# Performance work log

Hardware: AMD Instinct MI355X
Metric: run time of the kernel (lower is better)

## Reference

```python
import jax, jax.numpy as jnp
import numpy as np

HID = 1024; NH = 4; HD = HID // NH; KS = 4; C = 64; EPS = 1e-05
B = 4; L = 4096


def setup_inputs():
    key = jax.random.key(0)
    ks = jax.random.split(key, 9)
    return {
        "x": jax.random.normal(ks[0], (B, L, HID), jnp.float32),
        "Wq": jax.random.normal(ks[1], (HID, HID), jnp.float32) * 0.02,
        "Wk": jax.random.normal(ks[2], (HID, HID), jnp.float32) * 0.02,
        "Wv": jax.random.normal(ks[3], (HID, HID), jnp.float32) * 0.02,
        "Wb": jax.random.normal(ks[4], (HID, NH), jnp.float32) * 0.02,
        "conv_q": jax.random.normal(ks[5], (HID, 1, KS), jnp.float32) * 0.5,
        "conv_k": jax.random.normal(ks[6], (HID, 1, KS), jnp.float32) * 0.5,
        "conv_v": jax.random.normal(ks[7], (HID, 1, KS), jnp.float32) * 0.5,
        "g": jnp.ones((HD,), jnp.float32),
        "Wo": jax.random.normal(ks[8], (HID, HID), jnp.float32) * 0.02,
    }


def _causal_dwconv(x, w):
    # x: (B, L, Ch); w: (Ch, 1, K). Depthwise causal conv (left pad K-1) + SiLU,
    # equivalent to torch Conv1d(padding=K-1) followed by right-truncation.
    xc = jnp.moveaxis(x, 1, 2)  # (B, Ch, L)
    y = jax.lax.conv_general_dilated(
        xc, w, window_strides=(1,), padding=[(w.shape[-1] - 1, 0)],
        dimension_numbers=("NCH", "OIH", "NCH"), feature_group_count=w.shape[0])
    return jnp.moveaxis(jax.nn.silu(y), 1, 2)


def _forward(x, Wq, Wk, Wv, Wb, conv_q, conv_k, conv_v, g, Wo):
    Bx, Lx, _ = x.shape
    N = Lx // C  # num chunks (L chosen divisible by C)
    q = _causal_dwconv(x @ Wq, conv_q).reshape(Bx, Lx, NH, HD)
    k = _causal_dwconv(x @ Wk, conv_k).reshape(Bx, Lx, NH, HD)
    v = _causal_dwconv(x @ Wv, conv_v).reshape(Bx, Lx, NH, HD)
    # kq_norm: L2-normalize each head vector over head_dim
    q = q / jnp.linalg.norm(q, axis=-1, keepdims=True)
    k = k / jnp.linalg.norm(k, axis=-1, keepdims=True)
    beta = jax.nn.sigmoid(x @ Wb)  # (B, L, H)
    Q = q.reshape(Bx, N, C, NH, HD)
    K = k.reshape(Bx, N, C, NH, HD)
    V = v.reshape(Bx, N, C, NH, HD)
    bta = beta.reshape(Bx, N, C, NH, 1)
    Kb = K * bta
    Vb = V * bta
    # T = eye(C) - sum_h tril(Kb_h @ K_h^T, -1)  (T shared across heads, as in source)
    A = jnp.einsum("bnihd,bnjhd->bnij", Kb, K)
    T0 = jnp.eye(C, dtype=x.dtype) - jnp.tril(A, -1)
    col = jnp.arange(C)

    def body(i, T):
        # Replicates: T[:,:,i,:i] += (T[:,:,i,:,None] * T[:,:,:,:i]).sum(-2)
        row = jax.lax.dynamic_slice_in_dim(T, i, 1, axis=2)[:, :, 0]  # (B,N,C)
        acc = jnp.einsum("bnj,bnjc->bnc", row, T)
        new_row = jnp.where(col < i, row + acc, row)
        return jax.lax.dynamic_update_slice_in_dim(T, new_row[:, :, None, :], i, axis=2)

    T = jax.lax.fori_loop(1, C, body, T0)
    W = jnp.einsum("bnij,bnjhd->bnihd", T, Kb)
    U = jnp.einsum("bnij,bnjhd->bnihd", T, Vb)

    def chunk_step(S, inp):
        q_i, k_i, w_i, u0 = inp  # each (B, C, H, D)
        # source einsum 'bchd,bhdd->bchd' extracts the diagonal of S
        Sd = jnp.diagonal(S, axis1=-2, axis2=-1)  # (B, H, D)
        u_i = u0 - w_i * Sd[:, None]
        o_inter = q_i * Sd[:, None]
        # source: einsum('bchd,bchd->bc', q, k).tril() -- tril over the (B, C) matrix
        A_i = jnp.tril(jnp.einsum("bchd,bchd->bc", q_i, k_i))
        o_intra = A_i[:, :, None, None] * u_i
        S = S + jnp.einsum("bchd,bche->bhde", k_i, u_i)
        return S, o_inter + o_intra

    xs = tuple(jnp.moveaxis(a, 1, 0) for a in (Q, K, W, U))  # (N, B, C, H, D)
    S0 = jnp.zeros((Bx, NH, HD, HD), x.dtype)
    S, O = jax.lax.scan(chunk_step, S0, xs)
    o = jnp.moveaxis(O, 0, 1).reshape(Bx, Lx, NH, HD)
    # RMSNorm over head_dim with learned scale g
    o = o * jax.lax.rsqrt(jnp.mean(o * o, axis=-1, keepdims=True) + EPS) * g
    out = o.reshape(Bx, Lx, NH * HD) @ Wo
    return out, S


def reference(x, Wq, Wk, Wv, Wb, conv_q, conv_k, conv_v, g, Wo):
    return _forward(x, Wq, Wk, Wv, Wb, conv_q, conv_k, conv_v, g, Wo)
```

## Files before the change

### kernel.cpp

```cpp
#include <hip/hip_runtime.h>
#include <hip/hip_bf16.h>

#define HID 1024
#define NH 4
#define HD 256
#define NCH 64
#define BB 4
#define LL 4096
#define ROWS (BB*LL)
#define SSIZE (BB*NH*HD*HD)

typedef __hip_bfloat16 bf16;
typedef __attribute__((ext_vector_type(8))) short short8;
typedef __attribute__((ext_vector_type(4))) float f32x4;

struct u16x4 { unsigned short x, y, z, w; };

__device__ __forceinline__ float bfu2f(unsigned short u) {
  return __uint_as_float(((unsigned int)u) << 16);
}
__device__ __forceinline__ unsigned short f2bfu(float f) {
  unsigned int x = __float_as_uint(f);
  return (unsigned short)((x + 0x7FFFu + ((x >> 16) & 1u)) >> 16);
}
__device__ __forceinline__ float ldv(const float* p) { return *p; }
__device__ __forceinline__ float ldv(const bf16* p) { return bfu2f(*(const unsigned short*)p); }
__device__ __forceinline__ float4 ld4(const float* p) { return *(const float4*)p; }
__device__ __forceinline__ float4 ld4(const bf16* p) {
  u16x4 u = *(const u16x4*)p;
  return make_float4(bfu2f(u.x), bfu2f(u.y), bfu2f(u.z), bfu2f(u.w));
}
__device__ __forceinline__ void st4(float* p, float4 v) { *(float4*)p = v; }
__device__ __forceinline__ void st4(bf16* p, float4 v) {
  u16x4 u; u.x = f2bfu(v.x); u.y = f2bfu(v.y); u.z = f2bfu(v.z); u.w = f2bfu(v.w);
  *(u16x4*)p = u;
}

typedef const __attribute__((address_space(1))) unsigned int* gptr_t;
typedef __attribute__((address_space(3))) unsigned int* lptr_t;
__device__ __forceinline__ void gload16(const void* g, void* l) {
  __builtin_amdgcn_global_load_lds((gptr_t)g, (lptr_t)l, 16, 0, 0);
}

__global__ __launch_bounds__(256)
void beta_kernel(const float* __restrict__ x, const float* __restrict__ Wb,
                 float* __restrict__ beta) {
  const int wave = threadIdx.x >> 6, lane = threadIdx.x & 63;
  const int m = (blockIdx.x << 2) + wave;
  const float* xr = x + (size_t)m * HID;
  float a0 = 0.f, a1 = 0.f, a2 = 0.f, a3 = 0.f;
#pragma unroll
  for (int it = 0; it < 16; ++it) {
    int kk = lane + (it << 6);
    float xv = xr[kk];
    float4 w = *(const float4*)&Wb[kk << 2];
    a0 += xv * w.x; a1 += xv * w.y; a2 += xv * w.z; a3 += xv * w.w;
  }
#pragma unroll
  for (int off = 32; off; off >>= 1) {
    a0 += __shfl_xor(a0, off); a1 += __shfl_xor(a1, off);
    a2 += __shfl_xor(a2, off); a3 += __shfl_xor(a3, off);
  }
  if (lane == 0) {
    float4 r;
    r.x = 1.f / (1.f + expf(-a0)); r.y = 1.f / (1.f + expf(-a1));
    r.z = 1.f / (1.f + expf(-a2)); r.w = 1.f / (1.f + expf(-a3));
    *(float4*)&beta[m << 2] = r;
  }
}

__global__ __launch_bounds__(256)
void convX2_kernel(const float* __restrict__ x, bf16* __restrict__ hi,
                   bf16* __restrict__ lo) {
  size_t i = ((size_t)blockIdx.x * 256 + threadIdx.x) << 2;
  float4 v = *(const float4*)&x[i];
  u16x4 h; h.x = f2bfu(v.x); h.y = f2bfu(v.y); h.z = f2bfu(v.z); h.w = f2bfu(v.w);
  *(u16x4*)&hi[i] = h;
  u16x4 l;
  l.x = f2bfu(v.x - bfu2f(h.x)); l.y = f2bfu(v.y - bfu2f(h.y));
  l.z = f2bfu(v.z - bfu2f(h.z)); l.w = f2bfu(v.w - bfu2f(h.w));
  *(u16x4*)&lo[i] = l;
}

__global__ __launch_bounds__(256)
void convT_kernel(const float* __restrict__ W, unsigned short* __restrict__ Wt) {
  __shared__ unsigned short t[64][68];
  const int kt = blockIdx.x << 6, nt = blockIdx.y << 6;
  const int tid = threadIdx.x;
#pragma unroll
  for (int i = 0; i < 16; ++i) {
    int idx = tid + (i << 8);
    int r = idx >> 6, c = idx & 63;
    t[r][c] = f2bfu(W[(size_t)(kt + r) * HID + nt + c]);
  }
  __syncthreads();
#pragma unroll
  for (int i = 0; i < 16; ++i) {
    int idx = tid + (i << 8);
    int n = idx >> 6, kk = idx & 63;
    Wt[(size_t)(nt + n) * HID + kt + kk] = t[kk][n];
  }
}

__global__ __launch_bounds__(256)
void convT2_kernel(const float* __restrict__ W, unsigned short* __restrict__ Wht,
                   unsigned short* __restrict__ Wlt) {
  __shared__ float t[64][65];
  const int kt = blockIdx.x << 6, nt = blockIdx.y << 6;
  const int tid = threadIdx.x;
#pragma unroll
  for (int i = 0; i < 16; ++i) {
    int idx = tid + (i << 8);
    int r = idx >> 6, c = idx & 63;
    t[r][c] = W[(size_t)(kt + r) * HID + nt + c];
  }
  __syncthreads();
#pragma unroll
  for (int i = 0; i < 16; ++i) {
    int idx = tid + (i << 8);
    int n = idx >> 6, kk = idx & 63;
    float v = t[kk][n];
    unsigned short h = f2bfu(v);
    Wht[(size_t)(nt + n) * HID + kt + kk] = h;
    Wlt[(size_t)(nt + n) * HID + kt + kk] = f2bfu(v - bfu2f(h));
  }
}

__global__ __launch_bounds__(256)
void ktrans_kernel(const float* __restrict__ k, unsigned short* __restrict__ kt) {
  __shared__ float t[64][65];
  const int r0 = blockIdx.x << 6, c0 = blockIdx.y << 6;
  const int tid = threadIdx.x;
#pragma unroll
  for (int i = 0; i < 16; ++i) {
    int idx = tid + (i << 8);
    int rr = idx >> 6, cc = idx & 63;
    t[rr][cc] = k[(size_t)(r0 + rr) * HID + c0 + cc];
  }
  __syncthreads();
#pragma unroll
  for (int i = 0; i < 16; ++i) {
    int idx = tid + (i << 8);
    int cc = idx >> 6, rr = idx & 63;
    kt[(size_t)(c0 + cc) * ROWS + r0 + rr] = f2bfu(t[rr][cc]);
  }
}

__global__ __launch_bounds__(256)
void mfma_gemm(const unsigned short* __restrict__ A,
               const unsigned short* __restrict__ Bt, float* __restrict__ C) {
  __shared__ unsigned short Asl[128 * 32];
  __shared__ unsigned short Bsl[128 * 32];
  const int tid = threadIdx.x;
  const int wave = tid >> 6, lane = tid & 63;
  const int m0 = blockIdx.x << 7, n0 = blockIdx.y << 7;
  const int wr = wave >> 1, wc = wave & 1;
  f32x4 acc[4][4] = {};
  const int cA = (wave << 6) + lane;
  for (int k0 = 0; k0 < HID; k0 += 32) {
#pragma unroll
    for (int i = 0; i < 2; ++i) {
      int c = cA + (i << 8);
      int row = c >> 2, ko = (c & 3) << 3;
      gload16(&A[(size_t)(m0 + row) * HID + k0 + ko],
              &Asl[(size_t)((i << 8) + (wave << 6)) * 8]);
      gload16(&Bt[(size_t)(n0 + row) * HID + k0 + ko],
              &Bsl[(size_t)((i << 8) + (wave << 6)) * 8]);
    }
    __syncthreads();
    short8 af[4], bfr[4];
#pragma unroll
    for (int f = 0; f < 4; ++f) {
      int ra = (wr << 6) + (f << 4) + (lane & 15);
      af[f] = *(const short8*)&Asl[ra * 32 + ((lane >> 4) << 3)];
      int rb = (wc << 6) + (f << 4) + (lane & 15);
      bfr[f] = *(const short8*)&Bsl[rb * 32 + ((lane >> 4) << 3)];
    }
#pragma unroll
    for (int i = 0; i < 4; ++i)
#pragma unroll
      for (int j = 0; j < 4; ++j)
        acc[i][j] = __builtin_amdgcn_mfma_f32_16x16x32_bf16(af[i], bfr[j],
                                                            acc[i][j], 0, 0, 0);
    __syncthreads();
  }
#pragma unroll
  for (int i = 0; i < 4; ++i) {
    int r0 = m0 + (wr << 6) + (i << 4) + ((lane >> 4) << 2);
#pragma unroll
    for (int j = 0; j < 4; ++j) {
      int c0 = n0 + (wc << 6) + (j << 4) + (lane & 15);
#pragma unroll
      for (int r = 0; r < 4; ++r)
        C[(size_t)(r0 + r) * HID + c0] = acc[i][j][r];
    }
  }
}

__global__ __launch_bounds__(256)
void mfma_gemm3(const unsigned short* __restrict__ Ah_,
                const unsigned short* __restrict__ Al_,
                const unsigned short* __restrict__ Bh_,
                const unsigned short* __restrict__ Bl_,
                float* __restrict__ C) {
  __shared__ unsigned short Ah[128 * 32];
  __shared__ unsigned short Al[128 * 32];
  __shared__ unsigned short Bh[128 * 32];
  __shared__ unsigned short Bl[128 * 32];
  const int tid = threadIdx.x;
  const int wave = tid >> 6, lane = tid & 63;
  const int m0 = blockIdx.x << 7, n0 = blockIdx.y << 7;
  const int wr = wave >> 1, wc = wave & 1;
  f32x4 acc[4][4] = {};
  const int cA = (wave << 6) + lane;
  for (int k0 = 0; k0 < HID; k0 += 32) {
#pragma unroll
    for (int i = 0; i < 2; ++i) {
      int c = cA + (i << 8);
      int row = c >> 2, ko = (c & 3) << 3;
      size_t ga = (size_t)(m0 + row) * HID + k0 + ko;
      size_t gb = (size_t)(n0 + row) * HID + k0 + ko;
      size_t ldst = (size_t)((i << 8) + (wave << 6)) * 8;
      gload16(&Ah_[ga], &Ah[ldst]);
      gload16(&Al_[ga], &Al[ldst]);
      gload16(&Bh_[gb], &Bh[ldst]);
      gload16(&Bl_[gb], &Bl[ldst]);
    }
    __syncthreads();
    short8 ah[4], al[4], bh[4], bl[4];
#pragma unroll
    for (int f = 0; f < 4; ++f) {
      int ra = ((wr << 6) + (f << 4) + (lane & 15)) * 32 + ((lane >> 4) << 3);
      ah[f] = *(const short8*)&Ah[ra];
      al[f] = *(const short8*)&Al[ra];
      int rb = ((wc << 6) + (f << 4) + (lane & 15)) * 32 + ((lane >> 4) << 3);
      bh[f] = *(const short8*)&Bh[rb];
      bl[f] = *(const short8*)&Bl[rb];
    }
#pragma unroll
    for (int i = 0; i < 4; ++i)
#pragma unroll
      for (int j = 0; j < 4; ++j) {
        f32x4 a = acc[i][j];
        a = __builtin_amdgcn_mfma_f32_16x16x32_bf16(al[i], bh[j], a, 0, 0, 0);
        a = __builtin_amdgcn_mfma_f32_16x16x32_bf16(ah[i], bl[j], a, 0, 0, 0);
        a = __builtin_amdgcn_mfma_f32_16x16x32_bf16(ah[i], bh[j], a, 0, 0, 0);
        acc[i][j] = a;
      }
    __syncthreads();
  }
#pragma unroll
  for (int i = 0; i < 4; ++i) {
    int r0 = m0 + (wr << 6) + (i << 4) + ((lane >> 4) << 2);
#pragma unroll
    for (int j = 0; j < 4; ++j) {
      int c0 = n0 + (wc << 6) + (j << 4) + (lane & 15);
#pragma unroll
      for (int r = 0; r < 4; ++r)
        C[(size_t)(r0 + r) * HID + c0] = acc[i][j][r];
    }
  }
}

__global__ __launch_bounds__(256)
void mfma_gemmS(const unsigned short* __restrict__ At,
                const unsigned short* __restrict__ Bt,
                float* __restrict__ Spart, int ngroups) {
  __shared__ unsigned short Asl[128 * 32];
  __shared__ unsigned short Bsl[128 * 32];
  const int tid = threadIdx.x;
  const int wave = tid >> 6, lane = tid & 63;
  const int m0 = blockIdx.x << 7, n0 = blockIdx.y << 7;
  const int bh = blockIdx.z / ngroups;
  const int ng = blockIdx.z % ngroups;
  const int b = bh >> 2, h = bh & 3;
  const size_t kbase = (size_t)b * LL + (size_t)ng * (LL / ngroups);
  const int wr = wave >> 1, wc = wave & 1;
  f32x4 acc[4][4] = {};
  const int cA = (wave << 6) + lane;
  for (int k0 = 0; k0 < LL / ngroups; k0 += 32) {
#pragma unroll
    for (int i = 0; i < 2; ++i) {
      int c = cA + (i << 8);
      int row = c >> 2, ko = (c & 3) << 3;
      gload16(&At[((size_t)(h * HD + m0 + row)) * ROWS + kbase + k0 + ko],
              &Asl[(size_t)((i << 8) + (wave << 6)) * 8]);
      gload16(&Bt[((size_t)(bh * HD + n0 + row)) * LL + (size_t)ng * (LL / ngroups) + k0 + ko],
              &Bsl[(size_t)((i << 8) + (wave << 6)) * 8]);
    }
    __syncthreads();
    short8 af[4], bfr[4];
#pragma unroll
    for (int f = 0; f < 4; ++f) {
      int ra = (wr << 6) + (f << 4) + (lane & 15);
      af[f] = *(const short8*)&Asl[ra * 32 + ((lane >> 4) << 3)];
      int rb = (wc << 6) + (f << 4) + (lane & 15);
      bfr[f] = *(const short8*)&Bsl[rb * 32 + ((lane >> 4) << 3)];
    }
#pragma unroll
    for (int i = 0; i < 4; ++i)
#pragma unroll
      for (int j = 0; j < 4; ++j)
        acc[i][j] = __builtin_amdgcn_mfma_f32_16x16x32_bf16(af[i], bfr[j],
                                                            acc[i][j], 0, 0, 0);
    __syncthreads();
  }
  float* Cp = Spart + (size_t)ng * SSIZE + (size_t)bh * HD * HD;
#pragma unroll
  for (int i = 0; i < 4; ++i) {
    int r0 = m0 + (wr << 6) + (i << 4) + ((lane >> 4) << 2);
#pragma unroll
    for (int j = 0; j < 4; ++j) {
      int c0 = n0 + (wc << 6) + (j << 4) + (lane & 15);
#pragma unroll
      for (int r = 0; r < 4; ++r)
        Cp[(size_t)(r0 + r) * HD + c0] = acc[i][j][r];
    }
  }
}

template <int MODE, typename ST>
__global__ __launch_bounds__(256)
void conv_kernel(const float* __restrict__ lin, const float* __restrict__ w,
                 const float* __restrict__ beta, ST* __restrict__ out) {
  const int row = blockIdx.x;
  const int l = row & (LL - 1);
  const int tid = threadIdx.x;
  const int ch = tid << 2;
  float wv[4][4];
#pragma unroll
  for (int j = 0; j < 4; ++j) {
    float4 t4 = *(const float4*)&w[(ch + j) << 2];
    wv[j][0] = t4.x; wv[j][1] = t4.y; wv[j][2] = t4.z; wv[j][3] = t4.w;
  }
  float y[4] = {0.f, 0.f, 0.f, 0.f};
#pragma unroll
  for (int t = 0; t < 4; ++t) {
    if (l - 3 + t >= 0) {
      float4 xv = *(const float4*)&lin[(size_t)(row - 3 + t) * HID + ch];
      y[0] += xv.x * wv[0][t]; y[1] += xv.y * wv[1][t];
      y[2] += xv.z * wv[2][t]; y[3] += xv.w * wv[3][t];
    }
  }
#pragma unroll
  for (int j = 0; j < 4; ++j) y[j] = y[j] / (1.f + expf(-y[j]));
  float scale;
  if (MODE < 2) {
    float ss = y[0]*y[0] + y[1]*y[1] + y[2]*y[2] + y[3]*y[3];
#pragma unroll
    for (int off = 32; off; off >>= 1) ss += __shfl_xor(ss, off);
    scale = 1.f / sqrtf(ss);
  } else {
    scale = beta[(row << 2) + (tid >> 6)];
  }
  st4(&out[(size_t)row * HID + ch],
      make_float4(y[0]*scale, y[1]*scale, y[2]*scale, y[3]*scale));
}

__global__ __launch_bounds__(256)
void chunkT_kernel(const float* __restrict__ k, const float* __restrict__ beta,
                   float* __restrict__ Tg) {
  __shared__ float T[64][68];
  __shared__ float S1[64][68];
  __shared__ float S2[64][68];
  __shared__ float row_s[64];
  const int bn = blockIdx.x;
  const size_t base = (size_t)bn * 64 * HID;
  const int tid = threadIdx.x;
  const int tr = tid >> 4, tc = tid & 15;
  float acc[4][4] = {{0.f}};
  for (int d0 = 0; d0 < HID; d0 += 64) {
    const int h = d0 >> 8;
#pragma unroll
    for (int p = 0; p < 4; ++p) {
      int rr = (tid >> 4) + (p << 4);
      int c4 = (tid & 15) << 2;
      float4 a = *(const float4*)&k[base + (size_t)rr * HID + d0 + c4];
      float bta = beta[(((bn << 6) + rr) << 2) + h];
      S2[c4 + 0][rr] = a.x; S2[c4 + 1][rr] = a.y;
      S2[c4 + 2][rr] = a.z; S2[c4 + 3][rr] = a.w;
      S1[c4 + 0][rr] = a.x * bta; S1[c4 + 1][rr] = a.y * bta;
      S1[c4 + 2][rr] = a.z * bta; S1[c4 + 3][rr] = a.w * bta;
    }
    __syncthreads();
#pragma unroll
    for (int dd = 0; dd < 64; ++dd) {
      float4 a = *(const float4*)&S1[dd][tr << 2];
      float4 b = *(const float4*)&S2[dd][tc << 2];
      acc[0][0] += a.x*b.x; acc[0][1] += a.x*b.y; acc[0][2] += a.x*b.z; acc[0][3] += a.x*b.w;
      acc[1][0] += a.y*b.x; acc[1][1] += a.y*b.y; acc[1][2] += a.y*b.z; acc[1][3] += a.y*b.w;
      acc[2][0] += a.z*b.x; acc[2][1] += a.z*b.y; acc[2][2] += a.z*b.z; acc[2][3] += a.z*b.w;
      acc[3][0] += a.w*b.x; acc[3][1] += a.w*b.y; acc[3][2] += a.w*b.z; acc[3][3] += a.w*b.w;
    }
    __syncthreads();
  }
#pragma unroll
  for (int i = 0; i < 4; ++i)
#pragma unroll
    for (int j = 0; j < 4; ++j) {
      int ri = (tr << 2) + i, cj = (tc << 2) + j;
      T[ri][cj] = (ri == cj) ? 1.f : (ri > cj ? -acc[i][j] : 0.f);
    }
  __syncthreads();
  for (int i = 1; i < 64; ++i) {
    if (tid < 64) row_s[tid] = T[i][tid];
    __syncthreads();
    if (tid < 64) {
      float a = 0.f;
#pragma unroll 8
      for (int j = 0; j < 64; ++j) a += row_s[j] * T[j][tid];
      if (tid < i) T[i][tid] = row_s[tid] + a;
    }
    __syncthreads();
  }
#pragma unroll
  for (int ii = 0; ii < 4; ++ii) {
    int off = (tid << 4) + (ii << 2);
    int c = off >> 6, j = off & 63;
    *(float4*)&Tg[(size_t)bn * 4096 + off] = *(const float4*)&T[c][j];
  }
}

template <typename ST>
__global__ __launch_bounds__(256)
void prct_kernel(const float* __restrict__ k, const ST* __restrict__ v,
                 const float* __restrict__ beta, const float* __restrict__ Tg,
                 float* __restrict__ P, float* __restrict__ R) {
  __shared__ float Ts[4096];
  __shared__ float bs[64];
  const int bn = blockIdx.x >> 2, h = blockIdx.x & 3;
  const int tid = threadIdx.x;
#pragma unroll
  for (int ii = 0; ii < 4; ++ii) {
    int off = (tid << 4) + (ii << 2);
    *(float4*)&Ts[off] = *(const float4*)&Tg[(size_t)bn * 4096 + off];
  }
  if (tid < 64) bs[tid] = beta[(((bn << 6) + tid) << 2) + h];
  __syncthreads();
  const int ch = (h << 8) + tid;
  const size_t base = (size_t)bn * 64 * HID;
  float ct[64];
#pragma unroll
  for (int j = 0; j < 64; ++j) ct[j] = 0.f;
  for (int c = 0; c < 64; ++c) {
    float kc = k[base + (size_t)c * HID + ch];
#pragma unroll
    for (int j = 0; j < 64; ++j) ct[j] += Ts[(c << 6) + j] * kc;
  }
  float p = 0.f, r = 0.f;
#pragma unroll
  for (int j = 0; j < 64; ++j) {
    float kj = k[base + (size_t)j * HID + ch];
    float vj = ldv(&v[base + (size_t)j * HID + ch]);
    p += bs[j] * kj * ct[j];
    r += vj * ct[j];
  }
  P[(size_t)bn * HID + ch] = p;
  R[(size_t)bn * HID + ch] = r;
}

__global__ __launch_bounds__(256)
void scan_kernel(const float* __restrict__ P, const float* __restrict__ R,
                 float* __restrict__ Sdp) {
  const int b = blockIdx.x >> 2;
  const int ch = ((blockIdx.x & 3) << 8) + threadIdx.x;
  float S = 0.f;
  for (int n = 0; n < 64; ++n) {
    Sdp[(size_t)((n << 2) + b) * HID + ch] = S;
    float p = P[(size_t)((b << 6) + n) * HID + ch];
    float r = R[(size_t)((b << 6) + n) * HID + ch];
    S = S * (1.f - p) + r;
  }
}

template <typename ST>
__global__ __launch_bounds__(256)
void ai_kernel(const ST* __restrict__ q, const float* __restrict__ k,
               float* __restrict__ Ai) {
  const int bn = blockIdx.x;
  const int b = bn >> 6;
  const int wave = threadIdx.x >> 6, lane = threadIdx.x & 63;
  const size_t roff = ((size_t)bn * 64 + wave) * HID;
  float s = 0.f;
#pragma unroll
  for (int it = 0; it < 4; ++it) {
    int d = (lane << 2) + (it << 8);
    float4 a = ld4(&q[roff + d]);
    float4 b4 = *(const float4*)&k[roff + d];
    s += a.x*b4.x + a.y*b4.y + a.z*b4.z + a.w*b4.w;
  }
#pragma unroll
  for (int off = 32; off; off >>= 1) s += __shfl_xor(s, off);
  if (lane == 0) Ai[(bn << 2) + wave] = (wave <= b) ? s : 0.f;
}

__global__ __launch_bounds__(256)
void ucompute_kernel(const float* __restrict__ k, const bf16* __restrict__ v,
                     const float* __restrict__ beta, const float* __restrict__ Tg,
                     const float* __restrict__ Sdp, unsigned short* __restrict__ Ut) {
  __shared__ float Ts[4096];
  __shared__ float va[64][132];
  __shared__ float bs[64];
  const int bn = blockIdx.x >> 3;
  const int rr2 = blockIdx.x & 7;
  const int h = rr2 >> 1, eh = rr2 & 1;
  const int b = bn >> 6, nl = bn & 63;
  const int tid = threadIdx.x;
#pragma unroll
  for (int ii = 0; ii < 4; ++ii) {
    int off = (tid << 4) + (ii << 2);
    *(float4*)&Ts[off] = *(const float4*)&Tg[(size_t)bn * 4096 + off];
  }
  if (tid < 64) bs[tid] = beta[(((bn << 6) + tid) << 2) + h];
  __syncthreads();
  const size_t base = (size_t)bn * 64 * HID;
  const int ch0 = (h << 8) + (eh << 7);
#pragma unroll
  for (int p = 0; p < 8; ++p) {
    int idx = tid + (p << 8);
    int row = idx >> 5;
    int col4 = (idx & 31) << 2;
    int chg = ch0 + col4;
    float4 sd4 = *(const float4*)&Sdp[(size_t)((nl << 2) + b) * HID + chg];
    float4 k4 = *(const float4*)&k[base + (size_t)row * HID + chg];
    float4 v4 = ld4(&v[base + (size_t)row * HID + chg]);
    float bt = bs[row];
    va[row][col4 + 0] = v4.x - bt * k4.x * sd4.x;
    va[row][col4 + 1] = v4.y - bt * k4.y * sd4.y;
    va[row][col4 + 2] = v4.z - bt * k4.z * sd4.z;
    va[row][col4 + 3] = v4.w - bt * k4.w * sd4.w;
  }
  __syncthreads();
  const int e = tid & 127;
  const int chalf = tid >> 7;
  float acc[32];
#pragma unroll
  for (int c2 = 0; c2 < 32; ++c2) acc[c2] = 0.f;
  for (int j = 0; j < 64; ++j) {
    float vaj = va[j][e];
#pragma unroll
    for (int c2 = 0; c2 < 32; ++c2)
      acc[c2] += Ts[((chalf << 5) + c2) * 64 + j] * vaj;
  }
  const size_t ub = ((size_t)(((b << 2) + h) * HD) + (eh << 7) + e) * LL
                  + (nl << 6) + (chalf << 5);
#pragma unroll
  for (int c4 = 0; c4 < 8; ++c4) {
    u16x4 u;
    u.x = f2bfu(acc[(c4 << 2) + 0]); u.y = f2bfu(acc[(c4 << 2) + 1]);
    u.z = f2bfu(acc[(c4 << 2) + 2]); u.w = f2bfu(acc[(c4 << 2) + 3]);
    *(u16x4*)&Ut[ub + (c4 << 2)] = u;
  }
}

template <typename ST>
__global__ __launch_bounds__(256)
void o_kernel(ST* __restrict__ q, const float* __restrict__ Sdp,
              const unsigned short* __restrict__ Ut, const float* __restrict__ Ai,
              const float* __restrict__ g) {
  const int row = blockIdx.x;
  const int b = row >> 12;
  const int l = row & (LL - 1);
  const int n = l >> 6, c = l & 63;
  const int ch = threadIdx.x << 2;
  const size_t ro = (size_t)row * HID;
  float4 qv = ld4(&q[ro + ch]);
  float4 sd = *(const float4*)&Sdp[(size_t)((n << 2) + b) * HID + ch];
  float ox = qv.x*sd.x, oy = qv.y*sd.y, oz = qv.z*sd.z, ow = qv.w*sd.w;
  if (c <= b) {
    int bn = (b << 6) + n;
    float a = Ai[(bn << 2) + c];
    const int h = ch >> 8, e = ch & 255;
    const size_t ub = ((size_t)(((b << 2) + h) * HD) + e) * LL + (n << 6) + c;
    ox += a * bfu2f(Ut[ub + 0 * LL]);
    oy += a * bfu2f(Ut[ub + 1 * LL]);
    oz += a * bfu2f(Ut[ub + 2 * LL]);
    ow += a * bfu2f(Ut[ub + 3 * LL]);
  }
  float ss = ox*ox + oy*oy + oz*oz + ow*ow;
#pragma unroll
  for (int off = 32; off; off >>= 1) ss += __shfl_xor(ss, off);
  float scale = 1.f / sqrtf(ss * (1.f / HD) + 1e-5f);
  float4 gv = *(const float4*)&g[ch & (HD - 1)];
  st4(&q[ro + ch], make_float4(ox*scale*gv.x, oy*scale*gv.y, oz*scale*gv.z, ow*scale*gv.w));
}

__global__ __launch_bounds__(256)
void sreduce_kernel(const float* __restrict__ Spart, float* __restrict__ Sout,
                    int ngroups) {
  size_t i = ((size_t)blockIdx.x * 256 + threadIdx.x) << 2;
  float4 s = make_float4(0.f, 0.f, 0.f, 0.f);
  for (int g = 0; g < ngroups; ++g) {
    float4 p = *(const float4*)&Spart[(size_t)g * SSIZE + i];
    s.x += p.x; s.y += p.y; s.z += p.z; s.w += p.w;
  }
  *(float4*)&Sout[i] = s;
}

extern "C" void kernel_launch(void* const* d_in, const int* in_sizes, int n_in,
                              void* d_out, int out_size, void* d_ws, size_t ws_size,
                              hipStream_t stream) {
  const float* x  = (const float*)d_in[0];
  const float* Wq = (const float*)d_in[1];
  const float* Wk = (const float*)d_in[2];
  const float* Wv = (const float*)d_in[3];
  const float* Wb = (const float*)d_in[4];
  const float* cq = (const float*)d_in[5];
  const float* ck = (const float*)d_in[6];
  const float* cv = (const float*)d_in[7];
  const float* g  = (const float*)d_in[8];
  const float* Wo = (const float*)d_in[9];
  float* out  = (float*)d_out;
  float* Sout = out + (size_t)ROWS * HID;

  const size_t F = (size_t)ROWS * HID;
  char* w = (char*)d_ws;
  float* kbuf  = (float*)w;  w += F * 4;
  bf16*  xb    = (bf16*)w;   w += F * 2;
  bf16*  qbuf  = (bf16*)w;   w += F * 2;
  bf16*  vbuf  = (bf16*)w;   w += F * 2;
  unsigned short* Wqt  = (unsigned short*)w; w += (size_t)HID * HID * 2;
  unsigned short* Wvt  = (unsigned short*)w; w += (size_t)HID * HID * 2;
  unsigned short* Wot  = (unsigned short*)w; w += (size_t)HID * HID * 2;
  unsigned short* Wkht = (unsigned short*)w; w += (size_t)HID * HID * 2;
  unsigned short* Wklt = (unsigned short*)w; w += (size_t)HID * HID * 2;
  float* Tg    = (float*)w;  w += (size_t)BB * NCH * 4096 * 4;
  float* betab = (float*)w;  w += (size_t)ROWS * NH * 4;
  float* Aib   = (float*)w;  w += (size_t)BB * NCH * 4 * 4;
  float* Pb    = (float*)w;  w += (size_t)BB * NCH * HID * 4;
  float* Rb    = (float*)w;  w += (size_t)BB * NCH * HID * 4;
  float* Sdp   = (float*)w;  w += (size_t)BB * NCH * HID * 4;
  const size_t need = (size_t)(w - (char*)d_ws);
  if (ws_size < need) return;

  dim3 gg(ROWS / 128, HID / 128);
  dim3 gt(16, 16);
  float* lin = out;
  bf16* xlo = qbuf;

  convX2_kernel<<<F / 1024, 256, 0, stream>>>(x, xb, xlo);
  convT2_kernel<<<gt, 256, 0, stream>>>(Wk, Wkht, Wklt);
  convT_kernel<<<gt, 256, 0, stream>>>(Wq, Wqt);
  convT_kernel<<<gt, 256, 0, stream>>>(Wv, Wvt);
  convT_kernel<<<gt, 256, 0, stream>>>(Wo, Wot);
  beta_kernel<<<ROWS / 4, 256, 0, stream>>>(x, Wb, betab);

  mfma_gemm3<<<gg, 256, 0, stream>>>((const unsigned short*)xb,
                                     (const unsigned short*)xlo, Wkht, Wklt, lin);
  conv_kernel<1, float><<<ROWS, 256, 0, stream>>>(lin, ck, betab, kbuf);
  mfma_gemm<<<gg, 256, 0, stream>>>((const unsigned short*)xb, Wqt, lin);
  conv_kernel<0, bf16><<<ROWS, 256, 0, stream>>>(lin, cq, betab, qbuf);
  mfma_gemm<<<gg, 256, 0, stream>>>((const unsigned short*)xb, Wvt, lin);
  conv_kernel<2, bf16><<<ROWS, 256, 0, stream>>>(lin, cv, betab, vbuf);

  unsigned short* kt = (unsigned short*)xb;
  ktrans_kernel<<<dim3(ROWS / 64, HID / 64), 256, 0, stream>>>(kbuf, kt);

  chunkT_kernel<<<BB * NCH, 256, 0, stream>>>(kbuf, betab, Tg);
  prct_kernel<bf16><<<BB * NCH * NH, 256, 0, stream>>>(kbuf, vbuf, betab, Tg, Pb, Rb);
  scan_kernel<<<16, 256, 0, stream>>>(Pb, Rb, Sdp);
  ai_kernel<bf16><<<BB * NCH, 256, 0, stream>>>(qbuf, kbuf, Aib);

  unsigned short* Ut = (unsigned short*)lin;
  ucompute_kernel<<<BB * NCH * NH * 2, 256, 0, stream>>>(kbuf, vbuf, betab, Tg,
                                                         Sdp, Ut);
  o_kernel<bf16><<<ROWS, 256, 0, stream>>>(qbuf, Sdp, Ut, Aib, g);

  float* Spart = kbuf;
  const int ngroups = 8;
  mfma_gemmS<<<dim3(2, 2, 16 * ngroups), 256, 0, stream>>>(kt, Ut, Spart, ngroups);
  sreduce_kernel<<<SSIZE / 1024, 256, 0, stream>>>(Spart, Sout, ngroups);

  mfma_gemm<<<gg, 256, 0, stream>>>((const unsigned short*)qbuf, Wot, out);
}
```

Before: 846.6 us.

## Fuse prep kernels, emit bf16 GEMM intermediates, and process 8 rows per conv block

```diff
diff --git a/kernel.cpp b/kernel.cpp
--- a/kernel.cpp
+++ b/kernel.cpp
@@ -35,6 +35,10 @@
   u16x4 u; u.x = f2bfu(v.x); u.y = f2bfu(v.y); u.z = f2bfu(v.z); u.w = f2bfu(v.w);
   *(u16x4*)p = u;
 }
+__device__ __forceinline__ void stc(float* C, size_t i, float v) { C[i] = v; }
+__device__ __forceinline__ void stc(bf16* C, size_t i, float v) {
+  ((unsigned short*)C)[i] = f2bfu(v);
+}
 
 typedef const __attribute__((address_space(1))) unsigned int* gptr_t;
 typedef __attribute__((address_space(3))) unsigned int* lptr_t;
@@ -43,18 +47,30 @@
 }
 
 __global__ __launch_bounds__(256)
-void beta_kernel(const float* __restrict__ x, const float* __restrict__ Wb,
+void prep_kernel(const float* __restrict__ x, const float* __restrict__ Wb,
+                 bf16* __restrict__ hi, bf16* __restrict__ lo,
                  float* __restrict__ beta) {
   const int wave = threadIdx.x >> 6, lane = threadIdx.x & 63;
   const int m = (blockIdx.x << 2) + wave;
-  const float* xr = x + (size_t)m * HID;
   float a0 = 0.f, a1 = 0.f, a2 = 0.f, a3 = 0.f;
 #pragma unroll
-  for (int it = 0; it < 16; ++it) {
-    int kk = lane + (it << 6);
-    float xv = xr[kk];
-    float4 w = *(const float4*)&Wb[kk << 2];
-    a0 += xv * w.x; a1 += xv * w.y; a2 += xv * w.z; a3 += xv * w.w;
+  for (int it = 0; it < 4; ++it) {
+    int f4 = (it << 6) + lane;
+    size_t e = (size_t)m * 256 + f4;
+    float4 v = *(const float4*)&x[e << 2];
+    u16x4 h; h.x = f2bfu(v.x); h.y = f2bfu(v.y); h.z = f2bfu(v.z); h.w = f2bfu(v.w);
+    *(u16x4*)&hi[e << 2] = h;
+    u16x4 l;
+    l.x = f2bfu(v.x - bfu2f(h.x)); l.y = f2bfu(v.y - bfu2f(h.y));
+    l.z = f2bfu(v.z - bfu2f(h.z)); l.w = f2bfu(v.w - bfu2f(h.w));
+    *(u16x4*)&lo[e << 2] = l;
+    const float xs[4] = {v.x, v.y, v.z, v.w};
+#pragma unroll
+    for (int j = 0; j < 4; ++j) {
+      float4 wb = *(const float4*)&Wb[((f4 << 2) + j) << 2];
+      a0 += xs[j] * wb.x; a1 += xs[j] * wb.y;
+      a2 += xs[j] * wb.z; a3 += xs[j] * wb.w;
+    }
   }
 #pragma unroll
   for (int off = 32; off; off >>= 1) {
@@ -70,42 +86,14 @@
 }
 
 __global__ __launch_bounds__(256)
-void convX2_kernel(const float* __restrict__ x, bf16* __restrict__ hi,
-                   bf16* __restrict__ lo) {
-  size_t i = ((size_t)blockIdx.x * 256 + threadIdx.x) << 2;
-  float4 v = *(const float4*)&x[i];
-  u16x4 h; h.x = f2bfu(v.x); h.y = f2bfu(v.y); h.z = f2bfu(v.z); h.w = f2bfu(v.w);
-  *(u16x4*)&hi[i] = h;
-  u16x4 l;
-  l.x = f2bfu(v.x - bfu2f(h.x)); l.y = f2bfu(v.y - bfu2f(h.y));
-  l.z = f2bfu(v.z - bfu2f(h.z)); l.w = f2bfu(v.w - bfu2f(h.w));
-  *(u16x4*)&lo[i] = l;
-}
-
-__global__ __launch_bounds__(256)
-void convT_kernel(const float* __restrict__ W, unsigned short* __restrict__ Wt) {
-  __shared__ unsigned short t[64][68];
-  const int kt = blockIdx.x << 6, nt = blockIdx.y << 6;
-  const int tid = threadIdx.x;
-#pragma unroll
-  for (int i = 0; i < 16; ++i) {
-    int idx = tid + (i << 8);
-    int r = idx >> 6, c = idx & 63;
-    t[r][c] = f2bfu(W[(size_t)(kt + r) * HID + nt + c]);
-  }
-  __syncthreads();
-#pragma unroll
-  for (int i = 0; i < 16; ++i) {
-    int idx = tid + (i << 8);
-    int n = idx >> 6, kk = idx & 63;
-    Wt[(size_t)(nt + n) * HID + kt + kk] = t[kk][n];
-  }
-}
-
-__global__ __launch_bounds__(256)
-void convT2_kernel(const float* __restrict__ W, unsigned short* __restrict__ Wht,
-                   unsigned short* __restrict__ Wlt) {
+void convT_all(const float* __restrict__ Wq, const float* __restrict__ Wv,
+               const float* __restrict__ Wo, const float* __restrict__ Wk,
+               unsigned short* __restrict__ Wqt, unsigned short* __restrict__ Wvt,
+               unsigned short* __restrict__ Wot, unsigned short* __restrict__ Wkht,
+               unsigned short* __restrict__ Wklt) {
   __shared__ float t[64][65];
+  const int z = blockIdx.z;
+  const float* W = z == 0 ? Wq : z == 1 ? Wv : z == 2 ? Wo : Wk;
   const int kt = blockIdx.x << 6, nt = blockIdx.y << 6;
   const int tid = threadIdx.x;
 #pragma unroll
@@ -115,14 +103,24 @@
     t[r][c] = W[(size_t)(kt + r) * HID + nt + c];
   }
   __syncthreads();
-#pragma unroll
-  for (int i = 0; i < 16; ++i) {
-    int idx = tid + (i << 8);
-    int n = idx >> 6, kk = idx & 63;
-    float v = t[kk][n];
-    unsigned short h = f2bfu(v);
-    Wht[(size_t)(nt + n) * HID + kt + kk] = h;
-    Wlt[(size_t)(nt + n) * HID + kt + kk] = f2bfu(v - bfu2f(h));
+  if (z < 3) {
+    unsigned short* Wt = z == 0 ? Wqt : z == 1 ? Wvt : Wot;
+#pragma unroll
+    for (int i = 0; i < 16; ++i) {
+      int idx = tid + (i << 8);
+      int n = idx >> 6, kk = idx & 63;
+      Wt[(size_t)(nt + n) * HID + kt + kk] = f2bfu(t[kk][n]);
+    }
+  } else {
+#pragma unroll
+    for (int i = 0; i < 16; ++i) {
+      int idx = tid + (i << 8);
+      int n = idx >> 6, kk = idx & 63;
+      float v = t[kk][n];
+      unsigned short h = f2bfu(v);
+      Wkht[(size_t)(nt + n) * HID + kt + kk] = h;
+      Wklt[(size_t)(nt + n) * HID + kt + kk] = f2bfu(v - bfu2f(h));
+    }
   }
 }
 
@@ -146,9 +144,10 @@
   }
 }
 
+template <typename OT>
 __global__ __launch_bounds__(256)
 void mfma_gemm(const unsigned short* __restrict__ A,
-               const unsigned short* __restrict__ Bt, float* __restrict__ C) {
+               const unsigned short* __restrict__ Bt, OT* __restrict__ C) {
   __shared__ unsigned short Asl[128 * 32];
   __shared__ unsigned short Bsl[128 * 32];
   const int tid = threadIdx.x;
@@ -192,7 +191,7 @@
       int c0 = n0 + (wc << 6) + (j << 4) + (lane & 15);
 #pragma unroll
       for (int r = 0; r < 4; ++r)
-        C[(size_t)(r0 + r) * HID + c0] = acc[i][j][r];
+        stc(C, (size_t)(r0 + r) * HID + c0, acc[i][j][r]);
     }
   }
 }
@@ -319,42 +318,54 @@
   }
 }
 
-template <int MODE, typename ST>
-__global__ __launch_bounds__(256)
-void conv_kernel(const float* __restrict__ lin, const float* __restrict__ w,
-                 const float* __restrict__ beta, ST* __restrict__ out) {
-  const int row = blockIdx.x;
-  const int l = row & (LL - 1);
+template <int MODE, typename IT, typename ST>
+__global__ __launch_bounds__(256)
+void conv8_kernel(const IT* __restrict__ lin, const float* __restrict__ w,
+                  const float* __restrict__ beta, ST* __restrict__ out) {
+  const int row0 = blockIdx.x << 3;
   const int tid = threadIdx.x;
   const int ch = tid << 2;
+  const int h = tid >> 6;
   float wv[4][4];
 #pragma unroll
   for (int j = 0; j < 4; ++j) {
     float4 t4 = *(const float4*)&w[(ch + j) << 2];
     wv[j][0] = t4.x; wv[j][1] = t4.y; wv[j][2] = t4.z; wv[j][3] = t4.w;
   }
-  float y[4] = {0.f, 0.f, 0.f, 0.f};
-#pragma unroll
-  for (int t = 0; t < 4; ++t) {
-    if (l - 3 + t >= 0) {
-      float4 xv = *(const float4*)&lin[(size_t)(row - 3 + t) * HID + ch];
-      y[0] += xv.x * wv[0][t]; y[1] += xv.y * wv[1][t];
-      y[2] += xv.z * wv[2][t]; y[3] += xv.w * wv[3][t];
-    }
-  }
-#pragma unroll
-  for (int j = 0; j < 4; ++j) y[j] = y[j] / (1.f + expf(-y[j]));
-  float scale;
-  if (MODE < 2) {
-    float ss = y[0]*y[0] + y[1]*y[1] + y[2]*y[2] + y[3]*y[3];
-#pragma unroll
-    for (int off = 32; off; off >>= 1) ss += __shfl_xor(ss, off);
-    scale = 1.f / sqrtf(ss);
-  } else {
-    scale = beta[(row << 2) + (tid >> 6)];
-  }
-  st4(&out[(size_t)row * HID + ch],
-      make_float4(y[0]*scale, y[1]*scale, y[2]*scale, y[3]*scale));
+  const int l0 = row0 & (LL - 1);
+  const bool hasprev = (l0 != 0);
+  float4 xw0, xw1, xw2, xw3;
+  const float4 z4 = make_float4(0.f, 0.f, 0.f, 0.f);
+  xw0 = hasprev ? ld4(&lin[(size_t)(row0 - 3) * HID + ch]) : z4;
+  xw1 = hasprev ? ld4(&lin[(size_t)(row0 - 2) * HID + ch]) : z4;
+  xw2 = hasprev ? ld4(&lin[(size_t)(row0 - 1) * HID + ch]) : z4;
+#pragma unroll
+  for (int r = 0; r < 8; ++r) {
+    const int gr = row0 + r;
+    xw3 = ld4(&lin[(size_t)gr * HID + ch]);
+    float y[4];
+#pragma unroll
+    for (int j = 0; j < 4; ++j) {
+      float xv0 = j == 0 ? xw0.x : j == 1 ? xw0.y : j == 2 ? xw0.z : xw0.w;
+      float xv1 = j == 0 ? xw1.x : j == 1 ? xw1.y : j == 2 ? xw1.z : xw1.w;
+      float xv2 = j == 0 ? xw2.x : j == 1 ? xw2.y : j == 2 ? xw2.z : xw2.w;
+      float xv3 = j == 0 ? xw3.x : j == 1 ? xw3.y : j == 2 ? xw3.z : xw3.w;
+      y[j] = xv0 * wv[j][0] + xv1 * wv[j][1] + xv2 * wv[j][2] + xv3 * wv[j][3];
+      y[j] = y[j] / (1.f + expf(-y[j]));
+    }
+    float scale;
+    if (MODE < 2) {
+      float ss = y[0]*y[0] + y[1]*y[1] + y[2]*y[2] + y[3]*y[3];
+#pragma unroll
+      for (int off = 32; off; off >>= 1) ss += __shfl_xor(ss, off);
+      scale = 1.f / sqrtf(ss);
+    } else {
+      scale = beta[(gr << 2) + h];
+    }
+    st4(&out[(size_t)gr * HID + ch],
+        make_float4(y[0]*scale, y[1]*scale, y[2]*scale, y[3]*scale));
+    xw0 = xw1; xw1 = xw2; xw2 = xw3;
+  }
 }
 
 __global__ __launch_bounds__(256)
@@ -634,24 +645,21 @@
   if (ws_size < need) return;
 
   dim3 gg(ROWS / 128, HID / 128);
-  dim3 gt(16, 16);
-  float* lin = out;
-  bf16* xlo = qbuf;
-
-  convX2_kernel<<<F / 1024, 256, 0, stream>>>(x, xb, xlo);
-  convT2_kernel<<<gt, 256, 0, stream>>>(Wk, Wkht, Wklt);
-  convT_kernel<<<gt, 256, 0, stream>>>(Wq, Wqt);
-  convT_kernel<<<gt, 256, 0, stream>>>(Wv, Wvt);
-  convT_kernel<<<gt, 256, 0, stream>>>(Wo, Wot);
-  beta_kernel<<<ROWS / 4, 256, 0, stream>>>(x, Wb, betab);
+  float* linf = out;
+  bf16*  linb = (bf16*)out;
+  bf16*  xlo  = qbuf;
+
+  prep_kernel<<<ROWS / 4, 256, 0, stream>>>(x, Wb, xb, xlo, betab);
+  convT_all<<<dim3(16, 16, 4), 256, 0, stream>>>(Wq, Wv, Wo, Wk, Wqt, Wvt, Wot,
+                                                 Wkht, Wklt);
 
   mfma_gemm3<<<gg, 256, 0, stream>>>((const unsigned short*)xb,
-                                     (const unsigned short*)xlo, Wkht, Wklt, lin);
-  conv_kernel<1, float><<<ROWS, 256, 0, stream>>>(lin, ck, betab, kbuf);
-  mfma_gemm<<<gg, 256, 0, stream>>>((const unsigned short*)xb, Wqt, lin);
-  conv_kernel<0, bf16><<<ROWS, 256, 0, stream>>>(lin, cq, betab, qbuf);
-  mfma_gemm<<<gg, 256, 0, stream>>>((const unsigned short*)xb, Wvt, lin);
-  conv_kernel<2, bf16><<<ROWS, 256, 0, stream>>>(lin, cv, betab, vbuf);
+                                     (const unsigned short*)xlo, Wkht, Wklt, linf);
+  conv8_kernel<1, float, float><<<ROWS / 8, 256, 0, stream>>>(linf, ck, betab, kbuf);
+  mfma_gemm<bf16><<<gg, 256, 0, stream>>>((const unsigned short*)xb, Wqt, linb);
+  conv8_kernel<0, bf16, bf16><<<ROWS / 8, 256, 0, stream>>>(linb, cq, betab, qbuf);
+  mfma_gemm<bf16><<<gg, 256, 0, stream>>>((const unsigned short*)xb, Wvt, linb);
+  conv8_kernel<2, bf16, bf16><<<ROWS / 8, 256, 0, stream>>>(linb, cv, betab, vbuf);
 
   unsigned short* kt = (unsigned short*)xb;
   ktrans_kernel<<<dim3(ROWS / 64, HID / 64), 256, 0, stream>>>(kbuf, kt);
@@ -661,7 +669,7 @@
   scan_kernel<<<16, 256, 0, stream>>>(Pb, Rb, Sdp);
   ai_kernel<bf16><<<BB * NCH, 256, 0, stream>>>(qbuf, kbuf, Aib);
 
-  unsigned short* Ut = (unsigned short*)lin;
+  unsigned short* Ut = (unsigned short*)linb;
   ucompute_kernel<<<BB * NCH * NH * 2, 256, 0, stream>>>(kbuf, vbuf, betab, Tg,
                                                          Sdp, Ut);
   o_kernel<bf16><<<ROWS, 256, 0, stream>>>(qbuf, Sdp, Ut, Aib, g);
@@ -671,5 +679,5 @@
   mfma_gemmS<<<dim3(2, 2, 16 * ngroups), 256, 0, stream>>>(kt, Ut, Spart, ngroups);
   sreduce_kernel<<<SSIZE / 1024, 256, 0, stream>>>(Spart, Sout, ngroups);
 
-  mfma_gemm<<<gg, 256, 0, stream>>>((const unsigned short*)qbuf, Wot, out);
-}
+  mfma_gemm<float><<<gg, 256, 0, stream>>>((const unsigned short*)qbuf, Wot, out);
+}
```

Result: faster. 706.0 us (-16.6%).
